# Optimization experiments

Hardware: AMD Instinct MI355X
Metric: run time of the kernel (lower is better)

Reference implementation:

```python
import jax, jax.numpy as jnp
import numpy as np

N_NODES = 50000
N_EDGES = 1200000
BATCH = 64
D_IN = 2
D_EMB = 64
EPS = 1e-12


def _l2norm(x):
    # torch.nn.functional.normalize(dim=1): x / max(||x||_2, eps)
    n = jnp.sqrt(jnp.sum(x * x, axis=1, keepdims=True))
    return x / jnp.maximum(n, EPS)


def setup_inputs() -> dict:
    key = jax.random.key(0)
    ks = jax.random.split(key, 10)
    edge_row = jnp.sort(jax.random.randint(ks[0], (N_EDGES,), 0, N_NODES, dtype=jnp.int32))
    edge_col = jax.random.randint(ks[1], (N_EDGES,), 0, N_NODES, dtype=jnp.int32)
    batch_assign = jax.random.randint(ks[2], (N_NODES,), 0, BATCH, dtype=jnp.int32)
    input_features = jax.random.uniform(ks[3], (N_NODES, D_IN), dtype=jnp.float32)
    input_feature_s = jax.random.uniform(ks[4], (BATCH, D_IN), dtype=jnp.float32)
    W1 = jax.random.normal(ks[5], (D_IN, D_EMB), dtype=jnp.float32) * 0.1
    W2 = jax.random.normal(ks[6], (D_EMB, D_EMB), dtype=jnp.float32) * 0.1
    W3 = jax.random.normal(ks[7], (D_EMB, D_EMB), dtype=jnp.float32) * 0.1
    Wl = jax.random.normal(ks[8], (2 * D_EMB, D_EMB), dtype=jnp.float32) * 0.1
    bl = jnp.zeros((D_EMB,), dtype=jnp.float32)
    return {
        "edge_row": edge_row, "edge_col": edge_col, "batch_assign": batch_assign,
        "input_features": input_features, "input_feature_s": input_feature_s,
        "W1": W1, "W2": W2, "W3": W3, "Wl": Wl, "bl": bl, "depth": 3,
    }


def reference(edge_row, edge_col, batch_assign, input_features, input_feature_s,
              W1, W2, W3, Wl, bl, depth):
    n_nodes = input_features.shape[0]
    n_batch = input_feature_s.shape[0]

    h = _l2norm(jax.nn.relu(input_features @ W1))        # [N, d]
    hs = _l2norm(jax.nn.relu(input_feature_s @ W1))      # [B, d]

    for _ in range(depth):
        # SPMM node_node @ h : gather neighbor embeddings, sum per destination row
        h_nv = jax.ops.segment_sum(h[edge_col], edge_row, num_segments=n_nodes)  # [N, d]
        # SPMM batch_node @ h : pool node embeddings per graph
        h_nv_s = jax.ops.segment_sum(h, batch_assign, num_segments=n_batch)      # [B, d]
        h = _l2norm(jax.nn.relu(jnp.concatenate([h @ W2, h_nv @ W3], axis=1) @ Wl + bl))
        hs = _l2norm(jax.nn.relu(jnp.concatenate([hs @ W2, h_nv_s @ W3], axis=1) @ Wl + bl))
    return (h, hs)
```

## Files before the change

kernel.cpp:

```cpp
#include <hip/hip_runtime.h>
#include <math.h>

#define N_NODES 50000
#define N_EDGES 1200000
#define BATCH   64
#define D       64
#define EPS     1e-12f
#define NCOPY   64
#define PSZ     (NCOPY * BATCH * D)

#define EB  2344
#define MMB 8
#define IB  6258
#define NODE_BLOCKS 3125
#define HSB 4

__device__ __forceinline__ int rfl(int v) { return __builtin_amdgcn_readfirstlane(v); }

__global__ void __launch_bounds__(512) k_pro(const int* __restrict__ edge_row,
                                             int* __restrict__ row_start,
                                             float* __restrict__ PA, float* __restrict__ PB,
                                             const float* __restrict__ W2,
                                             const float* __restrict__ W3,
                                             const float* __restrict__ Wl,
                                             float* __restrict__ MM4,
                                             const float* __restrict__ X,
                                             const float* __restrict__ Xs,
                                             const float* __restrict__ W1,
                                             float* __restrict__ B0,
                                             float* __restrict__ HS) {
    int bid = blockIdx.x, t = threadIdx.x;
    if (bid < EB) {
        int tid = bid * 512 + t;
        for (int i = tid; i < PSZ; i += EB * 512) { PA[i] = 0.f; PB[i] = 0.f; }
        if (tid < N_EDGES) {
            int b = edge_row[tid];
            int a = (tid == 0) ? -1 : edge_row[tid - 1];
            for (int r = a + 1; r <= b; ++r) row_start[r] = tid;
            if (tid == N_EDGES - 1)
                for (int r = b + 1; r <= N_NODES; ++r) row_start[r] = N_EDGES;
        }
    } else if (bid < EB + MMB) {
        int k = (bid - EB) * 8 + (t >> 6), j = t & 63;
        float a2 = 0.f, a3 = 0.f;
        for (int q = 0; q < D; ++q) {
            a2 += W2[k*D + q] * Wl[q*D + j];
            a3 += W3[k*D + q] * Wl[(D + q)*D + j];
        }
        MM4[(k >> 1) * (D * 4) + j * 4 + (k & 1) * 2 + 0] = a2;
        MM4[(k >> 1) * (D * 4) + j * 4 + (k & 1) * 2 + 1] = a3;
    } else {
        int row = (bid - EB - MMB) * 8 + (t >> 6);
        int j = t & 63;
        if (row >= N_NODES + BATCH) return;
        float x0, x1; float* out;
        if (row < N_NODES) {
            x0 = X[row*2]; x1 = X[row*2 + 1]; out = B0 + (size_t)row * D;
        } else {
            int r = row - N_NODES;
            x0 = Xs[r*2]; x1 = Xs[r*2 + 1]; out = HS + (size_t)r * D;
        }
        float v = fmaxf(fmaf(x0, W1[j], x1 * W1[D + j]), 0.f);
        float ss = v * v;
        #pragma unroll
        for (int off = 32; off; off >>= 1) ss += __shfl_xor(ss, off);
        out[j] = v / fmaxf(sqrtf(ss), EPS);
    }
}

__global__ void __launch_bounds__(512, 8) k_iter(const int* __restrict__ edge_col,
                                                 const int* __restrict__ row_start,
                                                 const float* __restrict__ Hc,
                                                 float* __restrict__ Hn,
                                                 const float* __restrict__ MM4,
                                                 const float* __restrict__ bl,
                                                 const int* __restrict__ batch,
                                                 float* __restrict__ Pout,
                                                 float* __restrict__ HSrw,
                                                 float* __restrict__ Pin,
                                                 int hs_blocks) {
    __shared__ float4 sMM[32 * 64];
    __shared__ float4 sHG[8 * 64];
    int t = threadIdx.x, w = t >> 6, l = t & 63;
    const float4* gMM = (const float4*)MM4;
    for (int i = t; i < 2048; i += 512) sMM[i] = gMM[i];
    __syncthreads();

    int bid = blockIdx.x;
    bool is_hs = (bid < hs_blocks);
    int rA, rB;
    float hvA, hvB, gvA, gvB;

    if (!is_hs) {
        int pr = (bid - hs_blocks) * 8 + w;
        rA = 2 * pr; rB = rA + 1;
        int sA = rfl(row_start[rA]);
        int eA = rfl(row_start[rB]);
        int eB = rfl(row_start[rB + 1]);
        hvA = Hc[(size_t)rA * D + l];
        hvB = Hc[(size_t)rB * D + l];
        float aA = 0.f, aB = 0.f;
        int pad = 0;
        for (int base = sA; base < eB; ) {
            int cw = eB - base; if (cw > 64) cw = 64;
            int col = 0;
            if (l < cw) col = edge_col[base + l];
            int nb = (cw + 15) >> 4;
            pad += (nb << 4) - cw;
            for (int b = 0; b < nb; ++b) {
                #pragma unroll
                for (int u = 0; u < 16; ++u) {
                    int idx = (b << 4) + u;
                    int c = __builtin_amdgcn_readlane(col, idx);
                    const float* rp = Hc + (size_t)c * D;
                    float v = rp[l];
                    if (base + idx < eA) aA += v; else aB += v;
                }
            }
            base += cw;
        }
        aB -= (float)pad * Hc[l];
        gvA = aA; gvB = aB;
        float* cp = Pout + (size_t)(bid & (NCOPY - 1)) * (BATCH * D);
        int bA = rfl(batch[rA]);
        int bB = rfl(batch[rB]);
        atomicAdd(&cp[bA * D + l], hvA);
        atomicAdd(&cp[bB * D + l], hvB);
    } else {
        int pr = bid * 8 + w;
        rA = 2 * pr; rB = rA + 1;
        hvA = HSrw[(size_t)rA * D + l];
        hvB = HSrw[(size_t)rB * D + l];
        float aA = 0.f, aB = 0.f;
        #pragma unroll 4
        for (int c = 0; c < NCOPY; ++c) {
            float* p = Pin + (size_t)c * (BATCH * D) + rA * D + l;
            float vA = p[0], vB = p[D];
            p[0] = 0.f; p[D] = 0.f;
            aA += vA; aB += vB;
        }
        gvA = aA; gvB = aB;
    }

    sHG[w * 64 + l] = make_float4(hvA, hvB, gvA, gvB);
    float bj = bl[l];
    float a2x = 0.f, a2y = 0.f, a3x = bj, a3y = bj;
    const float4* hg = &sHG[w * 64];
    #pragma unroll
    for (int kk = 0; kk < 32; ++kk) {
        float4 mm = sMM[kk * 64 + l];
        float4 h0 = hg[2 * kk];
        float4 h1 = hg[2 * kk + 1];
        a2x = fmaf(h0.x, mm.x, a2x); a2y = fmaf(h0.y, mm.x, a2y);
        a3x = fmaf(h0.z, mm.y, a3x); a3y = fmaf(h0.w, mm.y, a3y);
        a2x = fmaf(h1.x, mm.z, a2x); a2y = fmaf(h1.y, mm.z, a2y);
        a3x = fmaf(h1.z, mm.w, a3x); a3y = fmaf(h1.w, mm.w, a3y);
    }
    float vA = fmaxf(a2x + a3x, 0.f);
    float vB = fmaxf(a2y + a3y, 0.f);
    float ssA = vA * vA, ssB = vB * vB;
    #pragma unroll
    for (int off = 32; off; off >>= 1) {
        ssA += __shfl_xor(ssA, off);
        ssB += __shfl_xor(ssB, off);
    }
    float oA = vA / fmaxf(sqrtf(ssA), EPS);
    float oB = vB / fmaxf(sqrtf(ssB), EPS);

    float* out = is_hs ? HSrw : Hn;
    out[(size_t)rA * D + l] = oA;
    out[(size_t)rB * D + l] = oB;
}

extern "C" void kernel_launch(void* const* d_in, const int* in_sizes, int n_in,
                              void* d_out, int out_size, void* d_ws, size_t ws_size,
                              hipStream_t stream) {
    const int*   edge_row = (const int*)  d_in[0];
    const int*   edge_col = (const int*)  d_in[1];
    const int*   batch    = (const int*)  d_in[2];
    const float* X        = (const float*)d_in[3];
    const float* Xs       = (const float*)d_in[4];
    const float* W1       = (const float*)d_in[5];
    const float* W2       = (const float*)d_in[6];
    const float* W3       = (const float*)d_in[7];
    const float* Wl       = (const float*)d_in[8];
    const float* bl       = (const float*)d_in[9];

    float* H  = (float*)d_out;
    float* HS = (float*)d_out + (size_t)N_NODES * D;

    float* B0  = (float*)d_ws;
    float* B1  = B0 + (size_t)N_NODES * D;
    float* PA  = B1 + (size_t)N_NODES * D;
    float* PB  = PA + PSZ;
    float* MM4 = PB + PSZ;
    int*   row_start = (int*)(MM4 + 32 * 64 * 4);

    k_pro<<<EB + MMB + IB, 512, 0, stream>>>(edge_row, row_start, PA, PB,
                                             W2, W3, Wl, MM4, X, Xs, W1, B0, HS);

    k_iter<<<NODE_BLOCKS, 512, 0, stream>>>(edge_col, row_start, B0, B1, MM4, bl,
                                            batch, PA, HS, PA, 0);
    k_iter<<<NODE_BLOCKS + HSB, 512, 0, stream>>>(edge_col, row_start, B1, B0, MM4, bl,
                                                  batch, PB, HS, PA, HSB);
    k_iter<<<NODE_BLOCKS + HSB, 512, 0, stream>>>(edge_col, row_start, B0, H, MM4, bl,
                                                  batch, PA, HS, PB, HSB);
    k_iter<<<HSB, 512, 0, stream>>>(edge_col, row_start, B0, B0, MM4, bl,
                                    batch, PB, HS, PA, HSB);
}
```

Measured before the change: 261.6 us.

## Use persistent waves with prefetch and fold batch pooling into fewer launches

Node blocks drop from one pair of rows per wave over 3125 blocks to a persistent grid of 768 blocks. Each wave loops over about four or five row pairs and prefetches the next pair's row_start, features, batch ids and first edge columns while it gathers the current pair. Pool accumulation moves into separate buffers. Pool partials for the next level are taken from both the input and the just-computed output embeddings, so the hs updates can apply two levels in one block and the fourth launch goes away. This trades occupancy for latency hiding and fewer launches, and it needs a third zeroed pool buffer.

```diff
diff --git a/kernel.cpp b/kernel.cpp
--- a/kernel.cpp
+++ b/kernel.cpp
@@ -12,14 +12,48 @@
 #define EB  2344
 #define MMB 8
 #define IB  6258
-#define NODE_BLOCKS 3125
+#define NB_NODE 768
+#define NWAVE   (NB_NODE * 8)
+#define NPAIR   25000
 #define HSB 4
 
 __device__ __forceinline__ int rfl(int v) { return __builtin_amdgcn_readfirstlane(v); }
+
+__device__ __forceinline__ int pair_of(int gw, int k) {
+    return (k < 4) ? (gw + k * NWAVE) : (4 * NWAVE + gw);
+}
+
+__device__ __forceinline__ void dense2(const float4* __restrict__ sMM,
+                                       float4* __restrict__ hg, int l,
+                                       float hvA, float hvB, float gvA, float gvB,
+                                       float bj, float& oA, float& oB) {
+    hg[l] = make_float4(hvA, hvB, gvA, gvB);
+    float a2x = 0.f, a2y = 0.f, a3x = bj, a3y = bj;
+    #pragma unroll
+    for (int kk = 0; kk < 32; ++kk) {
+        float4 mm = sMM[kk * 64 + l];
+        float4 h0 = hg[2 * kk];
+        float4 h1 = hg[2 * kk + 1];
+        a2x = fmaf(h0.x, mm.x, a2x); a2y = fmaf(h0.y, mm.x, a2y);
+        a3x = fmaf(h0.z, mm.y, a3x); a3y = fmaf(h0.w, mm.y, a3y);
+        a2x = fmaf(h1.x, mm.z, a2x); a2y = fmaf(h1.y, mm.z, a2y);
+        a3x = fmaf(h1.z, mm.w, a3x); a3y = fmaf(h1.w, mm.w, a3y);
+    }
+    float vA = fmaxf(a2x + a3x, 0.f);
+    float vB = fmaxf(a2y + a3y, 0.f);
+    float ssA = vA * vA, ssB = vB * vB;
+    #pragma unroll
+    for (int off = 32; off; off >>= 1) {
+        ssA += __shfl_xor(ssA, off);
+        ssB += __shfl_xor(ssB, off);
+    }
+    oA = vA / fmaxf(sqrtf(ssA), EPS);
+    oB = vB / fmaxf(sqrtf(ssB), EPS);
+}
 
 __global__ void __launch_bounds__(512) k_pro(const int* __restrict__ edge_row,
                                              int* __restrict__ row_start,
-                                             float* __restrict__ PA, float* __restrict__ PB,
+                                             float* __restrict__ PA,
                                              const float* __restrict__ W2,
                                              const float* __restrict__ W3,
                                              const float* __restrict__ Wl,
@@ -32,7 +66,7 @@
     int bid = blockIdx.x, t = threadIdx.x;
     if (bid < EB) {
         int tid = bid * 512 + t;
-        for (int i = tid; i < PSZ; i += EB * 512) { PA[i] = 0.f; PB[i] = 0.f; }
+        for (int i = tid; i < 3 * PSZ; i += EB * 512) PA[i] = 0.f;
         if (tid < N_EDGES) {
             int b = edge_row[tid];
             int a = (tid == 0) ? -1 : edge_row[tid - 1];
@@ -75,9 +109,11 @@
                                                  const float* __restrict__ MM4,
                                                  const float* __restrict__ bl,
                                                  const int* __restrict__ batch,
-                                                 float* __restrict__ Pout,
+                                                 float* __restrict__ PoolIn,
+                                                 float* __restrict__ PoolOut,
                                                  float* __restrict__ HSrw,
-                                                 float* __restrict__ Pin,
+                                                 const float* __restrict__ Pin1,
+                                                 const float* __restrict__ Pin2,
                                                  int hs_blocks) {
     __shared__ float4 sMM[32 * 64];
     __shared__ float4 sHG[8 * 64];
@@ -87,24 +123,73 @@
     __syncthreads();
 
     int bid = blockIdx.x;
-    bool is_hs = (bid < hs_blocks);
-    int rA, rB;
-    float hvA, hvB, gvA, gvB;
-
-    if (!is_hs) {
-        int pr = (bid - hs_blocks) * 8 + w;
-        rA = 2 * pr; rB = rA + 1;
-        int sA = rfl(row_start[rA]);
-        int eA = rfl(row_start[rB]);
-        int eB = rfl(row_start[rB + 1]);
-        hvA = Hc[(size_t)rA * D + l];
-        hvB = Hc[(size_t)rB * D + l];
+    float4* hg = &sHG[w * 64];
+    const float bj = bl[l];
+
+    if (bid < hs_blocks) {
+        int gwh = bid * 8 + w;
+        int rA = 2 * gwh, rB = rA + 1;
+        float hA = HSrw[(size_t)rA * D + l];
+        float hB = HSrw[(size_t)rB * D + l];
+        if (Pin1) {
+            float aA = 0.f, aB = 0.f;
+            #pragma unroll 4
+            for (int c = 0; c < NCOPY; ++c) {
+                const float* p = Pin1 + (size_t)c * (BATCH * D) + rA * D + l;
+                aA += p[0]; aB += p[D];
+            }
+            float oA, oB;
+            dense2(sMM, hg, l, hA, hB, aA, aB, bj, oA, oB);
+            hA = oA; hB = oB;
+        }
+        if (Pin2) {
+            float aA = 0.f, aB = 0.f;
+            #pragma unroll 4
+            for (int c = 0; c < NCOPY; ++c) {
+                const float* p = Pin2 + (size_t)c * (BATCH * D) + rA * D + l;
+                aA += p[0]; aB += p[D];
+            }
+            float oA, oB;
+            dense2(sMM, hg, l, hA, hB, aA, aB, bj, oA, oB);
+            hA = oA; hB = oB;
+        }
+        HSrw[(size_t)rA * D + l] = hA;
+        HSrw[(size_t)rB * D + l] = hB;
+        return;
+    }
+
+    const int gw = (bid - hs_blocks) * 8 + w;
+    const int npw = 4 + ((gw < NPAIR - 4 * NWAVE) ? 1 : 0);
+    const bool pool = (PoolIn != nullptr) || (PoolOut != nullptr);
+    const float h0l = Hc[l];
+
+    int p = gw;
+    int rs0 = row_start[2*p], rs1 = row_start[2*p+1], rs2 = row_start[2*p+2];
+    float hvA = Hc[(size_t)(2*p) * D + l];
+    float hvB = Hc[(size_t)(2*p) * D + D + l];
+    int bA = 0, bB = 0;
+    if (pool) { bA = batch[2*p]; bB = batch[2*p+1]; }
+    int sA = rfl(rs0), eA = rfl(rs1), eB2 = rfl(rs2);
+    int colv = 0;
+    { int ei = sA + l; if (ei < N_EDGES) colv = edge_col[ei]; }
+
+    for (int k = 0; k < npw; ++k) {
+        const bool hasnext = (k + 1 < npw);
+        int pn = p, rs0n = 0, rs1n = 0, rs2n = 0, bAn = 0, bBn = 0;
+        float hvAn = 0.f, hvBn = 0.f;
+        if (hasnext) {
+            pn = pair_of(gw, k + 1);
+            rs0n = row_start[2*pn]; rs1n = row_start[2*pn+1]; rs2n = row_start[2*pn+2];
+            hvAn = Hc[(size_t)(2*pn) * D + l];
+            hvBn = Hc[(size_t)(2*pn) * D + D + l];
+            if (pool) { bAn = batch[2*pn]; bBn = batch[2*pn+1]; }
+        }
         float aA = 0.f, aB = 0.f;
         int pad = 0;
-        for (int base = sA; base < eB; ) {
-            int cw = eB - base; if (cw > 64) cw = 64;
-            int col = 0;
-            if (l < cw) col = edge_col[base + l];
+        int cv = colv;
+        for (int base = sA; base < eB2; ) {
+            int cw = eB2 - base; if (cw > 64) cw = 64;
+            int col = (l < cw) ? cv : 0;
             int nb = (cw + 15) >> 4;
             pad += (nb << 4) - cw;
             for (int b = 0; b < nb; ++b) {
@@ -112,64 +197,43 @@
                 for (int u = 0; u < 16; ++u) {
                     int idx = (b << 4) + u;
                     int c = __builtin_amdgcn_readlane(col, idx);
-                    const float* rp = Hc + (size_t)c * D;
-                    float v = rp[l];
+                    float v = Hc[(size_t)c * D + l];
                     if (base + idx < eA) aA += v; else aB += v;
                 }
             }
             base += cw;
-        }
-        aB -= (float)pad * Hc[l];
-        gvA = aA; gvB = aB;
-        float* cp = Pout + (size_t)(bid & (NCOPY - 1)) * (BATCH * D);
-        int bA = rfl(batch[rA]);
-        int bB = rfl(batch[rB]);
-        atomicAdd(&cp[bA * D + l], hvA);
-        atomicAdd(&cp[bB * D + l], hvB);
-    } else {
-        int pr = bid * 8 + w;
-        rA = 2 * pr; rB = rA + 1;
-        hvA = HSrw[(size_t)rA * D + l];
-        hvB = HSrw[(size_t)rB * D + l];
-        float aA = 0.f, aB = 0.f;
-        #pragma unroll 4
-        for (int c = 0; c < NCOPY; ++c) {
-            float* p = Pin + (size_t)c * (BATCH * D) + rA * D + l;
-            float vA = p[0], vB = p[D];
-            p[0] = 0.f; p[D] = 0.f;
-            aA += vA; aB += vB;
-        }
-        gvA = aA; gvB = aB;
-    }
-
-    sHG[w * 64 + l] = make_float4(hvA, hvB, gvA, gvB);
-    float bj = bl[l];
-    float a2x = 0.f, a2y = 0.f, a3x = bj, a3y = bj;
-    const float4* hg = &sHG[w * 64];
-    #pragma unroll
-    for (int kk = 0; kk < 32; ++kk) {
-        float4 mm = sMM[kk * 64 + l];
-        float4 h0 = hg[2 * kk];
-        float4 h1 = hg[2 * kk + 1];
-        a2x = fmaf(h0.x, mm.x, a2x); a2y = fmaf(h0.y, mm.x, a2y);
-        a3x = fmaf(h0.z, mm.y, a3x); a3y = fmaf(h0.w, mm.y, a3y);
-        a2x = fmaf(h1.x, mm.z, a2x); a2y = fmaf(h1.y, mm.z, a2y);
-        a3x = fmaf(h1.z, mm.w, a3x); a3y = fmaf(h1.w, mm.w, a3y);
-    }
-    float vA = fmaxf(a2x + a3x, 0.f);
-    float vB = fmaxf(a2y + a3y, 0.f);
-    float ssA = vA * vA, ssB = vB * vB;
-    #pragma unroll
-    for (int off = 32; off; off >>= 1) {
-        ssA += __shfl_xor(ssA, off);
-        ssB += __shfl_xor(ssB, off);
-    }
-    float oA = vA / fmaxf(sqrtf(ssA), EPS);
-    float oB = vB / fmaxf(sqrtf(ssB), EPS);
-
-    float* out = is_hs ? HSrw : Hn;
-    out[(size_t)rA * D + l] = oA;
-    out[(size_t)rB * D + l] = oB;
+            if (base < eB2) {
+                int ei = base + l;
+                cv = (ei < N_EDGES) ? edge_col[ei] : 0;
+            }
+        }
+        aB -= (float)pad * h0l;
+
+        int sAn = 0, eAn = 0, eB2n = 0, colvn = 0;
+        if (hasnext) {
+            sAn = rfl(rs0n); eAn = rfl(rs1n); eB2n = rfl(rs2n);
+            int ei = sAn + l;
+            if (ei < N_EDGES) colvn = edge_col[ei];
+        }
+
+        int rA = 2 * p, rB = rA + 1;
+        if (PoolIn) {
+            float* cp = PoolIn + (size_t)(bid & (NCOPY - 1)) * (BATCH * D);
+            atomicAdd(&cp[rfl(bA) * D + l], hvA);
+            atomicAdd(&cp[rfl(bB) * D + l], hvB);
+        }
+        float oA, oB;
+        dense2(sMM, hg, l, hvA, hvB, aA, aB, bj, oA, oB);
+        Hn[(size_t)rA * D + l] = oA;
+        Hn[(size_t)rB * D + l] = oB;
+        if (PoolOut) {
+            float* cp = PoolOut + (size_t)(bid & (NCOPY - 1)) * (BATCH * D);
+            atomicAdd(&cp[rfl(bA) * D + l], oA);
+            atomicAdd(&cp[rfl(bB) * D + l], oB);
+        }
+        p = pn; sA = sAn; eA = eAn; eB2 = eB2n; colv = colvn;
+        hvA = hvAn; hvB = hvBn; bA = bAn; bB = bBn;
+    }
 }
 
 extern "C" void kernel_launch(void* const* d_in, const int* in_sizes, int n_in,
@@ -193,18 +257,17 @@
     float* B1  = B0 + (size_t)N_NODES * D;
     float* PA  = B1 + (size_t)N_NODES * D;
     float* PB  = PA + PSZ;
-    float* MM4 = PB + PSZ;
+    float* PC  = PB + PSZ;
+    float* MM4 = PC + PSZ;
     int*   row_start = (int*)(MM4 + 32 * 64 * 4);
 
-    k_pro<<<EB + MMB + IB, 512, 0, stream>>>(edge_row, row_start, PA, PB,
+    k_pro<<<EB + MMB + IB, 512, 0, stream>>>(edge_row, row_start, PA,
                                              W2, W3, Wl, MM4, X, Xs, W1, B0, HS);
 
-    k_iter<<<NODE_BLOCKS, 512, 0, stream>>>(edge_col, row_start, B0, B1, MM4, bl,
-                                            batch, PA, HS, PA, 0);
-    k_iter<<<NODE_BLOCKS + HSB, 512, 0, stream>>>(edge_col, row_start, B1, B0, MM4, bl,
-                                                  batch, PB, HS, PA, HSB);
-    k_iter<<<NODE_BLOCKS + HSB, 512, 0, stream>>>(edge_col, row_start, B0, H, MM4, bl,
-                                                  batch, PA, HS, PB, HSB);
-    k_iter<<<HSB, 512, 0, stream>>>(edge_col, row_start, B0, B0, MM4, bl,
-                                    batch, PB, HS, PA, HSB);
-}
+    k_iter<<<NB_NODE, 512, 0, stream>>>(edge_col, row_start, B0, B1, MM4, bl,
+                                        batch, PA, PB, HS, nullptr, nullptr, 0);
+    k_iter<<<NB_NODE + HSB, 512, 0, stream>>>(edge_col, row_start, B1, B0, MM4, bl,
+                                              batch, nullptr, PC, HS, PA, PB, HSB);
+    k_iter<<<NB_NODE + HSB, 512, 0, stream>>>(edge_col, row_start, B0, H, MM4, bl,
+                                              batch, nullptr, nullptr, HS, PC, nullptr, HSB);
+}
```

New measurement: 498.4 us. +90.5%, slower.
